# Kernel tuning notes

Hardware: AMD Instinct MI355X
Metric: run time of the kernel (lower is better)

Reference implementation:

```python
import jax, jax.numpy as jnp
import numpy as np
from jax import lax

C_IN, C_OUT, H, W = 64, 128, 512, 512


def setup_inputs() -> dict:
    key = jax.random.key(0)
    k1, k2, k3, k4 = jax.random.split(key, 4)
    x = jax.random.normal(k1, (C_IN, H, W), dtype=jnp.float32)
    # Conv2d params (eqx default: kernel 3x3, bias used). Small init scale for stability.
    conv_w = jax.random.normal(k2, (C_OUT, C_IN, 3, 3), dtype=jnp.float32) * 0.05
    conv_b = jax.random.normal(k3, (C_OUT,), dtype=jnp.float32) * 0.05
    fft_mask = jax.random.normal(k4, (C_OUT, H, W), dtype=jnp.float32)
    return {"x": x, "conv_w": conv_w, "conv_b": conv_b, "fft_mask": fft_mask}


def reference(x, conv_w, conv_b, fft_mask):
    # 3x3 same-padding conv on a single (C,H,W) sample -> (C_OUT,H,W)
    y = lax.conv_general_dilated(
        x[None],  # (1,C_IN,H,W)
        conv_w,
        window_strides=(1, 1),
        padding=((1, 1), (1, 1)),
        dimension_numbers=("NCHW", "OIHW", "NCHW"),
    )[0] + conv_b[:, None, None]
    # Per-channel spectral filter: FFT over (H,W), elementwise complex-mask
    # multiply, inverse FFT, take real part. Vectorized over channels.
    Y = jnp.fft.fftn(y, axes=(1, 2)) * fft_mask
    return jnp.fft.ifftn(Y, axes=(1, 2)).real
```

## Files before the change

kernel.cpp:

```cpp
#include <hip/hip_runtime.h>

#define CIN   64
#define COUT  128
#define HH    512
#define WW    512
#define HW    (HH*WW)

typedef __attribute__((ext_vector_type(8))) short  short8;
typedef __attribute__((ext_vector_type(4))) float  floatx4;


__device__ __forceinline__ unsigned short f2bf(float f) {
    unsigned u = __float_as_uint(f);
    u += 0x7fffu + ((u >> 16) & 1u);
    return (unsigned short)(u >> 16);
}

__device__ __forceinline__ void wave_sync() {
    __builtin_amdgcn_wave_barrier();
    asm volatile("s_waitcnt lgkmcnt(0)" ::: "memory");
    __builtin_amdgcn_sched_barrier(0);
}
template<bool BLK> __device__ __forceinline__ void xsync() {
    if (BLK) __syncthreads(); else wave_sync();
}


__global__ __launch_bounds__(256) void k_wprep(
        const float* __restrict__ cw,
        unsigned short* __restrict__ wt)
{
    int i = blockIdx.x * 256 + threadIdx.x;
    int tap = i >> 13;
    int co  = (i >> 6) & 127;
    int ci  = i & 63;
    wt[i] = f2bf(cw[(co * 64 + ci) * 9 + tap]);
}


__global__ __launch_bounds__(256) void k_xprep(
        const float* __restrict__ x,
        unsigned short* __restrict__ xt)
{
    __shared__ unsigned short tile[64][72];
    int t  = threadIdx.x;
    int h  = blockIdx.x >> 3;
    int w0 = (blockIdx.x & 7) << 6;
    int wl = t & 63;
#pragma unroll
    for (int it = 0; it < 16; ++it) {
        int ci = (t >> 6) + 4 * it;
        tile[wl][ci] = f2bf(x[ci * HW + h * 512 + w0 + wl]);
    }
    __syncthreads();
#pragma unroll
    for (int it = 0; it < 2; ++it) {
        int task = t + 256 * it;
        int w = task >> 3, seg = task & 7;
        *(short8*)&xt[((size_t)(h * 512 + w0 + w)) * 64 + seg * 8] =
            *(const short8*)&tile[w][seg * 8];
    }
}


__global__ __launch_bounds__(256) void k_maskT2(
        const float* __restrict__ mask,
        float* __restrict__ mt)
{
    __shared__ float t1[64][65];
    __shared__ float t2[64][65];
    int b  = blockIdx.x;
    int ch = b >> 6;
    int k0 = ((b >> 3) & 7) << 6;
    int c0 = (b & 7) << 6;
    int t  = threadIdx.x;
    int j  = t & 63, i0 = t >> 6;
    const float* mch = mask + (size_t)ch * HW;
#pragma unroll
    for (int it = 0; it < 16; ++it) {
        int i  = i0 + 4 * it;
        int mi = (512 - (k0 + i)) & 511;
        int mj = (512 - (c0 + j)) & 511;
        t1[i][j] = mch[(size_t)(k0 + i) * 512 + (c0 + j)];
        t2[i][j] = mch[(size_t)mi * 512 + mj];
    }
    __syncthreads();
    float* och = mt + (size_t)ch * HW;
#pragma unroll
    for (int it = 0; it < 16; ++it) {
        int jj = i0 + 4 * it;
        och[(size_t)(c0 + jj) * 512 + k0 + j] = t1[j][jj] + t2[j][jj];
    }
}


__global__ __launch_bounds__(512) void k_conv(
        const unsigned short* __restrict__ xt,
        const unsigned short* __restrict__ wt,
        const float* __restrict__ bias,
        float* __restrict__ y)
{
    __shared__ __align__(16) unsigned short As[3][130][68];

    int b  = blockIdx.x;
    int h  = b >> 2;
    int w0 = (b & 3) << 7;
    int t  = threadIdx.x;
    int lane = t & 63, wv = t >> 6;
    int wm = wv >> 2, wn = wv & 3;
    int l15 = lane & 15, quad = lane >> 4;

    for (int idx = t; idx < 3 * 130 * 8; idx += 512) {
        int dy  = idx / 1040;
        int rem = idx - dy * 1040;
        int p   = rem >> 3, seg = rem & 7;
        int hp  = h + dy - 1;
        int wq  = w0 - 1 + p;
        short8 v = {0, 0, 0, 0, 0, 0, 0, 0};
        if ((unsigned)hp < 512u && (unsigned)wq < 512u)
            v = *(const short8*)&xt[((size_t)(hp * 512 + wq)) * 64 + seg * 8];
        *(short8*)&As[dy][p][seg * 8] = v;
    }
    __syncthreads();

    floatx4 acc[4][2];
#pragma unroll
    for (int mt = 0; mt < 4; ++mt)
#pragma unroll
        for (int nt = 0; nt < 2; ++nt) {
            floatx4 z = {0.f, 0.f, 0.f, 0.f};
            acc[mt][nt] = z;
        }

#pragma unroll
    for (int tap = 0; tap < 9; ++tap) {
        int dy = tap / 3, dx = tap - dy * 3;
        short8 bfr[2][2];
#pragma unroll
        for (int nt = 0; nt < 2; ++nt)
#pragma unroll
            for (int kc = 0; kc < 2; ++kc) {
                int co = wn * 32 + nt * 16 + l15;
                bfr[nt][kc] = *(const short8*)
                    &wt[(tap * 128 + co) * 64 + kc * 32 + quad * 8];
            }
#pragma unroll
        for (int kc = 0; kc < 2; ++kc) {
            int c0 = kc * 32 + quad * 8;
            short8 afr[4];
#pragma unroll
            for (int mt = 0; mt < 4; ++mt) {
                int row = wm * 64 + mt * 16 + l15 + dx;
                afr[mt] = *(const short8*)&As[dy][row][c0];
            }
#pragma unroll
            for (int mt = 0; mt < 4; ++mt)
#pragma unroll
                for (int nt = 0; nt < 2; ++nt)
                    acc[mt][nt] = __builtin_amdgcn_mfma_f32_16x16x32_bf16(
                        afr[mt], bfr[nt][kc], acc[mt][nt], 0, 0, 0);
        }
    }

#pragma unroll
    for (int nt = 0; nt < 2; ++nt) {
        int co = wn * 32 + nt * 16 + l15;
        float bv = bias[co];
#pragma unroll
        for (int mt = 0; mt < 4; ++mt) {
            floatx4 o = acc[mt][nt];
            o[0] += bv; o[1] += bv; o[2] += bv; o[3] += bv;
            int m = wm * 64 + mt * 16 + quad * 4;
            *(floatx4*)&y[co * HW + h * 512 + w0 + m] = o;
        }
    }
}


#define FS 576

__device__ __forceinline__ int slotf(int c, int a) {
    return c * FS + ((a + (a >> 3)) ^ c);
}

__device__ __forceinline__ float2 cadd(float2 a, float2 b){ return make_float2(a.x+b.x, a.y+b.y); }
__device__ __forceinline__ float2 csub(float2 a, float2 b){ return make_float2(a.x-b.x, a.y-b.y); }

template<int DIR> __device__ __forceinline__ float2 twmul(float2 a, float2 t){
    return (DIR > 0) ? make_float2(a.x*t.x - a.y*t.y, a.x*t.y + a.y*t.x)
                     : make_float2(a.x*t.x + a.y*t.y, a.y*t.x - a.x*t.y);
}
template<int DIR> __device__ __forceinline__ float2 mulJ(float2 a){
    return (DIR > 0) ? make_float2(a.y, -a.x) : make_float2(-a.y, a.x);
}

#define RSQRT2 0.70710678118654752f

template<int DIR> __device__ __forceinline__ void dft8(float2* x){
    float2 a0 = cadd(x[0], x[4]), b0 = csub(x[0], x[4]);
    float2 a1 = cadd(x[1], x[5]), b1 = csub(x[1], x[5]);
    float2 a2 = cadd(x[2], x[6]), b2 = csub(x[2], x[6]);
    float2 a3 = cadd(x[3], x[7]), b3 = csub(x[3], x[7]);
    b1 = (DIR > 0) ? make_float2((b1.x + b1.y)*RSQRT2, (b1.y - b1.x)*RSQRT2)
                   : make_float2((b1.x - b1.y)*RSQRT2, (b1.y + b1.x)*RSQRT2);
    b2 = mulJ<DIR>(b2);
    b3 = (DIR > 0) ? make_float2((b3.y - b3.x)*RSQRT2, -(b3.x + b3.y)*RSQRT2)
                   : make_float2(-(b3.x + b3.y)*RSQRT2, (b3.x - b3.y)*RSQRT2);
    float2 c0 = cadd(a0, a2), d0 = csub(a0, a2);
    float2 c1 = cadd(a1, a3), d1 = mulJ<DIR>(csub(a1, a3));
    x[0] = cadd(c0, c1); x[4] = csub(c0, c1);
    x[2] = cadd(d0, d1); x[6] = csub(d0, d1);
    float2 e0 = cadd(b0, b2), f0 = csub(b0, b2);
    float2 e1 = cadd(b1, b3), f1 = mulJ<DIR>(csub(b1, b3));
    x[1] = cadd(e0, e1); x[5] = csub(e0, e1);
    x[3] = cadd(f0, f1); x[7] = csub(f0, f1);
}

template<bool BLK>
__device__ __forceinline__ void fft512_fwd(float2 X[4][8], float2* buf,
                                           const float2* tw, int w, int c) {
#pragma unroll
    for (int b = 0; b < 4; ++b) {
        dft8<1>(X[b]);
        int g = w + 16*b;
#pragma unroll
        for (int k = 1; k < 8; ++k) X[b][k] = twmul<1>(X[b][k], tw[g*k]);
    }
#pragma unroll
    for (int b = 0; b < 4; ++b) {
        int g = w + 16*b;
#pragma unroll
        for (int k = 0; k < 8; ++k) buf[slotf(c, k*64 + g)] = X[b][k];
    }
    xsync<BLK>();
#pragma unroll
    for (int b = 0; b < 4; ++b) {
        int u = w + 16*b; int bs = (u >> 3)*64 + (u & 7);
#pragma unroll
        for (int g2 = 0; g2 < 8; ++g2) X[b][g2] = buf[slotf(c, bs + 8*g2)];
    }
#pragma unroll
    for (int b = 0; b < 4; ++b) {
        dft8<1>(X[b]);
        int g1 = (w + 16*b) & 7;
#pragma unroll
        for (int k = 1; k < 8; ++k) X[b][k] = twmul<1>(X[b][k], tw[8*g1*k]);
    }
    xsync<BLK>();
#pragma unroll
    for (int b = 0; b < 4; ++b) {
        int u = w + 16*b; int bs = (u >> 3)*64 + (u & 7);
#pragma unroll
        for (int k = 0; k < 8; ++k) buf[slotf(c, bs + 8*k)] = X[b][k];
    }
    xsync<BLK>();
#pragma unroll
    for (int b = 0; b < 4; ++b) {
        int v = w + 16*b;
#pragma unroll
        for (int g1 = 0; g1 < 8; ++g1) X[b][g1] = buf[slotf(c, 8*v + g1)];
    }
#pragma unroll
    for (int b = 0; b < 4; ++b) dft8<1>(X[b]);
}

template<bool BLK>
__device__ __forceinline__ void fft512_inv(float2 X[4][8], float2* buf,
                                           const float2* tw, int w, int c) {
#pragma unroll
    for (int b = 0; b < 4; ++b) dft8<-1>(X[b]);
    xsync<BLK>();
#pragma unroll
    for (int b = 0; b < 4; ++b) {
        int v = w + 16*b;
#pragma unroll
        for (int g1 = 0; g1 < 8; ++g1) buf[slotf(c, 8*v + g1)] = X[b][g1];
    }
    xsync<BLK>();
#pragma unroll
    for (int b = 0; b < 4; ++b) {
        int u = w + 16*b; int bs = (u >> 3)*64 + (u & 7);
#pragma unroll
        for (int k = 0; k < 8; ++k) X[b][k] = buf[slotf(c, bs + 8*k)];
    }
#pragma unroll
    for (int b = 0; b < 4; ++b) {
        int g1 = (w + 16*b) & 7;
#pragma unroll
        for (int k = 1; k < 8; ++k) X[b][k] = twmul<-1>(X[b][k], tw[8*g1*k]);
        dft8<-1>(X[b]);
    }
    xsync<BLK>();
#pragma unroll
    for (int b = 0; b < 4; ++b) {
        int u = w + 16*b; int bs = (u >> 3)*64 + (u & 7);
#pragma unroll
        for (int g2 = 0; g2 < 8; ++g2) buf[slotf(c, bs + 8*g2)] = X[b][g2];
    }
    xsync<BLK>();
#pragma unroll
    for (int b = 0; b < 4; ++b) {
        int g = w + 16*b;
#pragma unroll
        for (int k = 0; k < 8; ++k) X[b][k] = buf[slotf(c, k*64 + g)];
    }
#pragma unroll
    for (int b = 0; b < 4; ++b) {
        int g = w + 16*b;
#pragma unroll
        for (int k = 1; k < 8; ++k) X[b][k] = twmul<-1>(X[b][k], tw[g*k]);
        dft8<-1>(X[b]);
    }
}

__device__ __forceinline__ void build_tw(float2* tw, int t) {
    const float a0 = -6.283185307179586f / 512.0f;
    float s, c;
    __sincosf(a0 * (float)t, &s, &c);         tw[t]       = make_float2(c, s);
    __sincosf(a0 * (float)(t + 256), &s, &c); tw[t + 256] = make_float2(c, s);
}


__global__ __launch_bounds__(256) void k_rows_fwd_pair(
        const float* __restrict__ y,
        float2* __restrict__ Z)
{
    __shared__ float2 buf[16 * FS];
    __shared__ float2 tw[512];
    int t = threadIdx.x;
    build_tw(tw, t);
    int c = t >> 4, w = t & 15;
    int p = blockIdx.x >> 5, r0 = (blockIdx.x & 31) << 4;
    const float* yA = y + (size_t)(2*p) * HW;
    const float* yB = yA + HW;

    for (int it = 0; it < 16; ++it) {
        int n = t + 256*it;
        int rr = n >> 8, q = n & 255;
        float2 a2 = *(const float2*)&yA[(size_t)(r0 + rr)*512 + 2*q];
        float2 b2 = *(const float2*)&yB[(size_t)(r0 + rr)*512 + 2*q];
        buf[slotf(rr, 2*q)]     = make_float2(a2.x, b2.x);
        buf[slotf(rr, 2*q + 1)] = make_float2(a2.y, b2.y);
    }
    __syncthreads();
    float2 X[4][8];
#pragma unroll
    for (int b = 0; b < 4; ++b)
#pragma unroll
        for (int r = 0; r < 8; ++r)
            X[b][r] = buf[slotf(c, w + 16*b + 64*r)];
    wave_sync();
    fft512_fwd<false>(X, buf, tw, w, c);

    wave_sync();
#pragma unroll
    for (int b = 0; b < 4; ++b) {
        int v = w + 16*b; int kb = (v >> 3) + 8*(v & 7);
#pragma unroll
        for (int m = 0; m < 8; ++m) buf[slotf(c, kb + 64*m)] = X[b][m];
    }
    __syncthreads();
    size_t zb = (size_t)p * HW + r0;
    for (int it = 0; it < 32; ++it) {
        int n = t + 256*it;
        int col = n >> 4, rr = n & 15;
        Z[zb + (size_t)col*512 + rr] = buf[slotf(rr, col)];
    }
}

__device__ __forceinline__ int col_of(int g, int j) {
    if (g == 0) return (j < 8) ? j : (j == 8 ? 256 : 496 + j);
    return (j < 8) ? 8*g + j : 512 - 8*g - 15 + j;
}
__device__ __forceinline__ int jmir(int g, int j) {
    return (g == 0) ? ((16 - j) & 15) : (15 - j);
}

__global__ __launch_bounds__(256) void k_cols_pair(
        float2* __restrict__ Z,
        const float* __restrict__ mt)
{
    __shared__ float2 buf[16 * FS];
    __shared__ float2 tw[512];
    int t = threadIdx.x;
    build_tw(tw, t);
    int c = t >> 4, w = t & 15;
    int p = blockIdx.x >> 5, g = blockIdx.x & 31;
    int colc = col_of(g, c);
    int cm   = jmir(g, c);
    size_t zch = (size_t)p * HW;
    const float* mAp = mt + (size_t)(2*p) * HW + (size_t)colc * 512;
    const float* mBp = mAp + HW;

    for (int it = 0; it < 32; ++it) {
        int n = t + 256*it;
        int cj = n >> 9, row = n & 511;
        buf[slotf(cj, row)] = Z[zch + (size_t)col_of(g, cj)*512 + row];
    }
    float Sa[4][8], Sb[4][8];
#pragma unroll
    for (int b = 0; b < 4; ++b) {
        int v = w + 16*b; int kb = (v >> 3) + 8*(v & 7);
#pragma unroll
        for (int m = 0; m < 8; ++m) {
            int k1 = kb + 64*m;
            Sa[b][m] = mAp[k1];
            Sb[b][m] = mBp[k1];
        }
    }
    __syncthreads();
    float2 X[4][8];
#pragma unroll
    for (int b = 0; b < 4; ++b)
#pragma unroll
        for (int r = 0; r < 8; ++r)
            X[b][r] = buf[slotf(c, w + 16*b + 64*r)];
    wave_sync();
    fft512_fwd<false>(X, buf, tw, w, c);

    wave_sync();
#pragma unroll
    for (int b = 0; b < 4; ++b) {
        int v = w + 16*b; int kb = (v >> 3) + 8*(v & 7);
#pragma unroll
        for (int m = 0; m < 8; ++m) buf[slotf(c, kb + 64*m)] = X[b][m];
    }
    __syncthreads();

    const float s4 = 0.25f / 262144.0f;
#pragma unroll
    for (int b = 0; b < 4; ++b) {
        int v = w + 16*b; int kb = (v >> 3) + 8*(v & 7);
#pragma unroll
        for (int m = 0; m < 8; ++m) {
            int k1  = kb + 64*m;
            int mk1 = (512 - k1) & 511;
            float2 P = X[b][m];
            float2 Q = buf[slotf(cm, mk1)];
            float alpha = (Sa[b][m] + Sb[b][m]) * s4;
            float beta  = (Sa[b][m] - Sb[b][m]) * s4;
            X[b][m] = make_float2(alpha * P.x + beta * Q.x,
                                  alpha * P.y - beta * Q.y);
        }
    }
    __syncthreads();
    fft512_inv<false>(X, buf, tw, w, c);
    wave_sync();
#pragma unroll
    for (int b = 0; b < 4; ++b)
#pragma unroll
        for (int r = 0; r < 8; ++r)
            buf[slotf(c, w + 16*b + 64*r)] = X[b][r];
    __syncthreads();
    for (int it = 0; it < 32; ++it) {
        int n = t + 256*it;
        int cj = n >> 9, row = n & 511;
        Z[zch + (size_t)col_of(g, cj)*512 + row] = buf[slotf(cj, row)];
    }
}

__global__ __launch_bounds__(256) void k_rows_inv_pair(
        const float2* __restrict__ Z,
        float* __restrict__ out)
{
    __shared__ float2 buf[16 * FS];
    __shared__ float2 tw[512];
    int t = threadIdx.x;
    build_tw(tw, t);
    int c = t >> 4, w = t & 15;
    int p = blockIdx.x >> 5, r0 = (blockIdx.x & 31) << 4;
    size_t zb = (size_t)p * HW + r0;

    for (int it = 0; it < 32; ++it) {
        int n = t + 256*it;
        int col = n >> 4, rr = n & 15;
        buf[slotf(rr, col)] = Z[zb + (size_t)col*512 + rr];
    }
    __syncthreads();

    float2 X[4][8];
#pragma unroll
    for (int b = 0; b < 4; ++b) {
        int v = w + 16*b; int kb = (v >> 3) + 8*(v & 7);
#pragma unroll
        for (int m = 0; m < 8; ++m) X[b][m] = buf[slotf(c, kb + 64*m)];
    }
    fft512_inv<false>(X, buf, tw, w, c);
    wave_sync();
#pragma unroll
    for (int b = 0; b < 4; ++b)
#pragma unroll
        for (int r = 0; r < 8; ++r)
            buf[slotf(c, w + 16*b + 64*r)] = X[b][r];
    __syncthreads();
    float* oA = out + (size_t)(2*p) * HW;
    float* oB = oA + HW;
    for (int it = 0; it < 16; ++it) {
        int n = t + 256*it;
        int rr = n >> 8, q = n & 255;
        float2 v0 = buf[slotf(rr, 2*q)];
        float2 v1 = buf[slotf(rr, 2*q + 1)];
        *(float2*)&oA[(size_t)(r0 + rr)*512 + 2*q] = make_float2(v0.x, v1.x);
        *(float2*)&oB[(size_t)(r0 + rr)*512 + 2*q] = make_float2(v0.y, v1.y);
    }
}


extern "C" void kernel_launch(void* const* d_in, const int* in_sizes, int n_in,
                              void* d_out, int out_size, void* d_ws, size_t ws_size,
                              hipStream_t stream) {
    const float* x    = (const float*)d_in[0];
    const float* cw   = (const float*)d_in[1];
    const float* cb   = (const float*)d_in[2];
    const float* mask = (const float*)d_in[3];

    float*  outRe = (float*)d_out;
    float2* ZT    = (float2*)d_ws;

    unsigned short* xt = (unsigned short*)d_ws;
    unsigned short* wt = (unsigned short*)d_ws + (size_t)HW * 64;

    k_wprep<<<288, 256, 0, stream>>>(cw, wt);
    k_xprep<<<4096, 256, 0, stream>>>(x, xt);
    k_conv<<<2048, 512, 0, stream>>>(xt, wt, cb, outRe);
    k_rows_fwd_pair<<<2048, 256, 0, stream>>>(outRe, ZT);
    k_maskT2<<<8192, 256, 0, stream>>>(mask, outRe);
    k_cols_pair<<<2048, 256, 0, stream>>>(ZT, outRe);
    k_rows_inv_pair<<<2048, 256, 0, stream>>>(ZT, outRe);
}
```

Measured before the change: 631.1 us.

## Halve FFT rows per block and load/store FFT data directly from global memory

The three FFT kernels now give each block 8 rows (32 threads per row, 16 elements per thread) instead of 16, so shared memory and register use per block roughly halve and launch bounds request 4 blocks per CU. The grid doubles to 4096 blocks. The first-stage loads and final stores now go straight between registers and global memory, skipping the shared-memory staging pass where the access pattern allows it. The risks are less coalesced global accesses for the strided per-thread pattern, and more blocks that each rebuild the twiddle table.

```diff
diff --git a/kernel.cpp b/kernel.cpp
--- a/kernel.cpp
+++ b/kernel.cpp
@@ -181,6 +181,9 @@
 
 __device__ __forceinline__ int slotf(int c, int a) {
     return c * FS + ((a + (a >> 3)) ^ c);
+}
+__device__ __forceinline__ int dr6(int v) {
+    return (v >> 3) + 8 * (v & 7);
 }
 
 __device__ __forceinline__ float2 cadd(float2 a, float2 b){ return make_float2(a.x+b.x, a.y+b.y); }
@@ -217,96 +220,96 @@
 }
 
 template<bool BLK>
-__device__ __forceinline__ void fft512_fwd(float2 X[4][8], float2* buf,
+__device__ __forceinline__ void fft512_fwd(float2 X[2][8], float2* buf,
                                            const float2* tw, int w, int c) {
 #pragma unroll
-    for (int b = 0; b < 4; ++b) {
+    for (int b = 0; b < 2; ++b) {
         dft8<1>(X[b]);
-        int g = w + 16*b;
+        int g = w + 32*b;
 #pragma unroll
         for (int k = 1; k < 8; ++k) X[b][k] = twmul<1>(X[b][k], tw[g*k]);
     }
 #pragma unroll
-    for (int b = 0; b < 4; ++b) {
-        int g = w + 16*b;
+    for (int b = 0; b < 2; ++b) {
+        int g = w + 32*b;
 #pragma unroll
         for (int k = 0; k < 8; ++k) buf[slotf(c, k*64 + g)] = X[b][k];
     }
     xsync<BLK>();
 #pragma unroll
-    for (int b = 0; b < 4; ++b) {
-        int u = w + 16*b; int bs = (u >> 3)*64 + (u & 7);
+    for (int b = 0; b < 2; ++b) {
+        int u = w + 32*b; int bs = (u >> 3)*64 + (u & 7);
 #pragma unroll
         for (int g2 = 0; g2 < 8; ++g2) X[b][g2] = buf[slotf(c, bs + 8*g2)];
     }
 #pragma unroll
-    for (int b = 0; b < 4; ++b) {
+    for (int b = 0; b < 2; ++b) {
         dft8<1>(X[b]);
-        int g1 = (w + 16*b) & 7;
+        int g1 = (w + 32*b) & 7;
 #pragma unroll
         for (int k = 1; k < 8; ++k) X[b][k] = twmul<1>(X[b][k], tw[8*g1*k]);
     }
     xsync<BLK>();
 #pragma unroll
-    for (int b = 0; b < 4; ++b) {
-        int u = w + 16*b; int bs = (u >> 3)*64 + (u & 7);
+    for (int b = 0; b < 2; ++b) {
+        int u = w + 32*b; int bs = (u >> 3)*64 + (u & 7);
 #pragma unroll
         for (int k = 0; k < 8; ++k) buf[slotf(c, bs + 8*k)] = X[b][k];
     }
     xsync<BLK>();
 #pragma unroll
-    for (int b = 0; b < 4; ++b) {
-        int v = w + 16*b;
+    for (int b = 0; b < 2; ++b) {
+        int v = w + 32*b;
 #pragma unroll
         for (int g1 = 0; g1 < 8; ++g1) X[b][g1] = buf[slotf(c, 8*v + g1)];
     }
 #pragma unroll
-    for (int b = 0; b < 4; ++b) dft8<1>(X[b]);
+    for (int b = 0; b < 2; ++b) dft8<1>(X[b]);
 }
 
 template<bool BLK>
-__device__ __forceinline__ void fft512_inv(float2 X[4][8], float2* buf,
+__device__ __forceinline__ void fft512_inv(float2 X[2][8], float2* buf,
                                            const float2* tw, int w, int c) {
 #pragma unroll
-    for (int b = 0; b < 4; ++b) dft8<-1>(X[b]);
-    xsync<BLK>();
-#pragma unroll
-    for (int b = 0; b < 4; ++b) {
-        int v = w + 16*b;
+    for (int b = 0; b < 2; ++b) dft8<-1>(X[b]);
+    xsync<BLK>();
+#pragma unroll
+    for (int b = 0; b < 2; ++b) {
+        int v = w + 32*b;
 #pragma unroll
         for (int g1 = 0; g1 < 8; ++g1) buf[slotf(c, 8*v + g1)] = X[b][g1];
     }
     xsync<BLK>();
 #pragma unroll
-    for (int b = 0; b < 4; ++b) {
-        int u = w + 16*b; int bs = (u >> 3)*64 + (u & 7);
+    for (int b = 0; b < 2; ++b) {
+        int u = w + 32*b; int bs = (u >> 3)*64 + (u & 7);
 #pragma unroll
         for (int k = 0; k < 8; ++k) X[b][k] = buf[slotf(c, bs + 8*k)];
     }
 #pragma unroll
-    for (int b = 0; b < 4; ++b) {
-        int g1 = (w + 16*b) & 7;
+    for (int b = 0; b < 2; ++b) {
+        int g1 = (w + 32*b) & 7;
 #pragma unroll
         for (int k = 1; k < 8; ++k) X[b][k] = twmul<-1>(X[b][k], tw[8*g1*k]);
         dft8<-1>(X[b]);
     }
     xsync<BLK>();
 #pragma unroll
-    for (int b = 0; b < 4; ++b) {
-        int u = w + 16*b; int bs = (u >> 3)*64 + (u & 7);
+    for (int b = 0; b < 2; ++b) {
+        int u = w + 32*b; int bs = (u >> 3)*64 + (u & 7);
 #pragma unroll
         for (int g2 = 0; g2 < 8; ++g2) buf[slotf(c, bs + 8*g2)] = X[b][g2];
     }
     xsync<BLK>();
 #pragma unroll
-    for (int b = 0; b < 4; ++b) {
-        int g = w + 16*b;
+    for (int b = 0; b < 2; ++b) {
+        int g = w + 32*b;
 #pragma unroll
         for (int k = 0; k < 8; ++k) X[b][k] = buf[slotf(c, k*64 + g)];
     }
 #pragma unroll
-    for (int b = 0; b < 4; ++b) {
-        int g = w + 16*b;
+    for (int b = 0; b < 2; ++b) {
+        int g = w + 32*b;
 #pragma unroll
         for (int k = 1; k < 8; ++k) X[b][k] = twmul<-1>(X[b][k], tw[g*k]);
         dft8<-1>(X[b]);
@@ -321,86 +324,80 @@
 }
 
 
-__global__ __launch_bounds__(256) void k_rows_fwd_pair(
+__global__ __launch_bounds__(256, 4) void k_rows_fwd_pair(
         const float* __restrict__ y,
         float2* __restrict__ Z)
 {
-    __shared__ float2 buf[16 * FS];
+    __shared__ float2 buf[8 * FS];
     __shared__ float2 tw[512];
     int t = threadIdx.x;
     build_tw(tw, t);
-    int c = t >> 4, w = t & 15;
-    int p = blockIdx.x >> 5, r0 = (blockIdx.x & 31) << 4;
-    const float* yA = y + (size_t)(2*p) * HW;
+    int c = t >> 5, w = t & 31;
+    int p = blockIdx.x >> 6, r0 = (blockIdx.x & 63) << 3;
+    const float* yA = y + (size_t)(2*p) * HW + (size_t)(r0 + c) * 512;
     const float* yB = yA + HW;
 
+    float2 X[2][8];
+#pragma unroll
+    for (int b = 0; b < 2; ++b)
+#pragma unroll
+        for (int r = 0; r < 8; ++r) {
+            int off = w + 32*b + 64*r;
+            X[b][r] = make_float2(yA[off], yB[off]);
+        }
+    __syncthreads();
+    fft512_fwd<false>(X, buf, tw, w, c);
+
+    wave_sync();
+#pragma unroll
+    for (int b = 0; b < 2; ++b) {
+        int kb = dr6(w + 32*b);
+#pragma unroll
+        for (int m = 0; m < 8; ++m) buf[slotf(c, kb + 64*m)] = X[b][m];
+    }
+    __syncthreads();
+    size_t zb = (size_t)p * HW + r0;
     for (int it = 0; it < 16; ++it) {
         int n = t + 256*it;
-        int rr = n >> 8, q = n & 255;
-        float2 a2 = *(const float2*)&yA[(size_t)(r0 + rr)*512 + 2*q];
-        float2 b2 = *(const float2*)&yB[(size_t)(r0 + rr)*512 + 2*q];
-        buf[slotf(rr, 2*q)]     = make_float2(a2.x, b2.x);
-        buf[slotf(rr, 2*q + 1)] = make_float2(a2.y, b2.y);
-    }
-    __syncthreads();
-    float2 X[4][8];
-#pragma unroll
-    for (int b = 0; b < 4; ++b)
-#pragma unroll
-        for (int r = 0; r < 8; ++r)
-            X[b][r] = buf[slotf(c, w + 16*b + 64*r)];
-    wave_sync();
-    fft512_fwd<false>(X, buf, tw, w, c);
-
-    wave_sync();
-#pragma unroll
-    for (int b = 0; b < 4; ++b) {
-        int v = w + 16*b; int kb = (v >> 3) + 8*(v & 7);
-#pragma unroll
-        for (int m = 0; m < 8; ++m) buf[slotf(c, kb + 64*m)] = X[b][m];
-    }
-    __syncthreads();
-    size_t zb = (size_t)p * HW + r0;
-    for (int it = 0; it < 32; ++it) {
-        int n = t + 256*it;
-        int col = n >> 4, rr = n & 15;
+        int col = n >> 3, rr = n & 7;
         Z[zb + (size_t)col*512 + rr] = buf[slotf(rr, col)];
     }
 }
 
 __device__ __forceinline__ int col_of(int g, int j) {
-    if (g == 0) return (j < 8) ? j : (j == 8 ? 256 : 496 + j);
-    return (j < 8) ? 8*g + j : 512 - 8*g - 15 + j;
+    if (g == 0) return (j < 4) ? j : (j == 4 ? 256 : 504 + j);
+    return (j < 4) ? 4*g + j : 512 - 4*g - 7 + j;
 }
 __device__ __forceinline__ int jmir(int g, int j) {
-    return (g == 0) ? ((16 - j) & 15) : (15 - j);
-}
-
-__global__ __launch_bounds__(256) void k_cols_pair(
+    return (g == 0) ? ((8 - j) & 7) : (7 - j);
+}
+
+__global__ __launch_bounds__(256, 4) void k_cols_pair(
         float2* __restrict__ Z,
         const float* __restrict__ mt)
 {
-    __shared__ float2 buf[16 * FS];
+    __shared__ float2 buf[8 * FS];
     __shared__ float2 tw[512];
     int t = threadIdx.x;
     build_tw(tw, t);
-    int c = t >> 4, w = t & 15;
-    int p = blockIdx.x >> 5, g = blockIdx.x & 31;
+    int c = t >> 5, w = t & 31;
+    int p = blockIdx.x >> 6, g = blockIdx.x & 63;
     int colc = col_of(g, c);
     int cm   = jmir(g, c);
-    size_t zch = (size_t)p * HW;
+    size_t zcol = (size_t)p * HW + (size_t)colc * 512;
     const float* mAp = mt + (size_t)(2*p) * HW + (size_t)colc * 512;
     const float* mBp = mAp + HW;
 
-    for (int it = 0; it < 32; ++it) {
-        int n = t + 256*it;
-        int cj = n >> 9, row = n & 511;
-        buf[slotf(cj, row)] = Z[zch + (size_t)col_of(g, cj)*512 + row];
-    }
-    float Sa[4][8], Sb[4][8];
-#pragma unroll
-    for (int b = 0; b < 4; ++b) {
-        int v = w + 16*b; int kb = (v >> 3) + 8*(v & 7);
+    float2 X[2][8];
+#pragma unroll
+    for (int b = 0; b < 2; ++b)
+#pragma unroll
+        for (int r = 0; r < 8; ++r)
+            X[b][r] = Z[zcol + w + 32*b + 64*r];
+    float Sa[2][8], Sb[2][8];
+#pragma unroll
+    for (int b = 0; b < 2; ++b) {
+        int kb = dr6(w + 32*b);
 #pragma unroll
         for (int m = 0; m < 8; ++m) {
             int k1 = kb + 64*m;
@@ -409,19 +406,12 @@
         }
     }
     __syncthreads();
-    float2 X[4][8];
-#pragma unroll
-    for (int b = 0; b < 4; ++b)
-#pragma unroll
-        for (int r = 0; r < 8; ++r)
-            X[b][r] = buf[slotf(c, w + 16*b + 64*r)];
+    fft512_fwd<false>(X, buf, tw, w, c);
+
     wave_sync();
-    fft512_fwd<false>(X, buf, tw, w, c);
-
-    wave_sync();
-#pragma unroll
-    for (int b = 0; b < 4; ++b) {
-        int v = w + 16*b; int kb = (v >> 3) + 8*(v & 7);
+#pragma unroll
+    for (int b = 0; b < 2; ++b) {
+        int kb = dr6(w + 32*b);
 #pragma unroll
         for (int m = 0; m < 8; ++m) buf[slotf(c, kb + 64*m)] = X[b][m];
     }
@@ -429,8 +419,8 @@
 
     const float s4 = 0.25f / 262144.0f;
 #pragma unroll
-    for (int b = 0; b < 4; ++b) {
-        int v = w + 16*b; int kb = (v >> 3) + 8*(v & 7);
+    for (int b = 0; b < 2; ++b) {
+        int kb = dr6(w + 32*b);
 #pragma unroll
         for (int m = 0; m < 8; ++m) {
             int k1  = kb + 64*m;
@@ -445,64 +435,51 @@
     }
     __syncthreads();
     fft512_inv<false>(X, buf, tw, w, c);
-    wave_sync();
-#pragma unroll
-    for (int b = 0; b < 4; ++b)
+#pragma unroll
+    for (int b = 0; b < 2; ++b)
 #pragma unroll
         for (int r = 0; r < 8; ++r)
-            buf[slotf(c, w + 16*b + 64*r)] = X[b][r];
-    __syncthreads();
-    for (int it = 0; it < 32; ++it) {
-        int n = t + 256*it;
-        int cj = n >> 9, row = n & 511;
-        Z[zch + (size_t)col_of(g, cj)*512 + row] = buf[slotf(cj, row)];
-    }
-}
-
-__global__ __launch_bounds__(256) void k_rows_inv_pair(
+            Z[zcol + w + 32*b + 64*r] = X[b][r];
+}
+
+__global__ __launch_bounds__(256, 4) void k_rows_inv_pair(
         const float2* __restrict__ Z,
         float* __restrict__ out)
 {
-    __shared__ float2 buf[16 * FS];
+    __shared__ float2 buf[8 * FS];
     __shared__ float2 tw[512];
     int t = threadIdx.x;
     build_tw(tw, t);
-    int c = t >> 4, w = t & 15;
-    int p = blockIdx.x >> 5, r0 = (blockIdx.x & 31) << 4;
+    int c = t >> 5, w = t & 31;
+    int p = blockIdx.x >> 6, r0 = (blockIdx.x & 63) << 3;
     size_t zb = (size_t)p * HW + r0;
 
-    for (int it = 0; it < 32; ++it) {
-        int n = t + 256*it;
-        int col = n >> 4, rr = n & 15;
-        buf[slotf(rr, col)] = Z[zb + (size_t)col*512 + rr];
-    }
-    __syncthreads();
-
-    float2 X[4][8];
-#pragma unroll
-    for (int b = 0; b < 4; ++b) {
-        int v = w + 16*b; int kb = (v >> 3) + 8*(v & 7);
-#pragma unroll
-        for (int m = 0; m < 8; ++m) X[b][m] = buf[slotf(c, kb + 64*m)];
-    }
-    fft512_inv<false>(X, buf, tw, w, c);
-    wave_sync();
-#pragma unroll
-    for (int b = 0; b < 4; ++b)
-#pragma unroll
-        for (int r = 0; r < 8; ++r)
-            buf[slotf(c, w + 16*b + 64*r)] = X[b][r];
-    __syncthreads();
-    float* oA = out + (size_t)(2*p) * HW;
-    float* oB = oA + HW;
     for (int it = 0; it < 16; ++it) {
         int n = t + 256*it;
-        int rr = n >> 8, q = n & 255;
-        float2 v0 = buf[slotf(rr, 2*q)];
-        float2 v1 = buf[slotf(rr, 2*q + 1)];
-        *(float2*)&oA[(size_t)(r0 + rr)*512 + 2*q] = make_float2(v0.x, v1.x);
-        *(float2*)&oB[(size_t)(r0 + rr)*512 + 2*q] = make_float2(v0.y, v1.y);
-    }
+        int col = n >> 3, rr = n & 7;
+        buf[slotf(rr, col)] = Z[zb + (size_t)col*512 + rr];
+    }
+    __syncthreads();
+
+    float2 X[2][8];
+#pragma unroll
+    for (int b = 0; b < 2; ++b) {
+        int kb = dr6(w + 32*b);
+#pragma unroll
+        for (int m = 0; m < 8; ++m) X[b][m] = buf[slotf(c, kb + 64*m)];
+    }
+    fft512_inv<false>(X, buf, tw, w, c);
+
+    float* oA = out + (size_t)(2*p) * HW + (size_t)(r0 + c) * 512;
+    float* oB = oA + HW;
+#pragma unroll
+    for (int b = 0; b < 2; ++b)
+#pragma unroll
+        for (int r = 0; r < 8; ++r) {
+            int off = w + 32*b + 64*r;
+            oA[off] = X[b][r].x;
+            oB[off] = X[b][r].y;
+        }
 }
 
 
@@ -523,8 +500,8 @@
     k_wprep<<<288, 256, 0, stream>>>(cw, wt);
     k_xprep<<<4096, 256, 0, stream>>>(x, xt);
     k_conv<<<2048, 512, 0, stream>>>(xt, wt, cb, outRe);
-    k_rows_fwd_pair<<<2048, 256, 0, stream>>>(outRe, ZT);
+    k_rows_fwd_pair<<<4096, 256, 0, stream>>>(outRe, ZT);
     k_maskT2<<<8192, 256, 0, stream>>>(mask, outRe);
-    k_cols_pair<<<2048, 256, 0, stream>>>(ZT, outRe);
-    k_rows_inv_pair<<<2048, 256, 0, stream>>>(ZT, outRe);
-}
+    k_cols_pair<<<4096, 256, 0, stream>>>(ZT, outRe);
+    k_rows_inv_pair<<<4096, 256, 0, stream>>>(ZT, outRe);
+}
```

Result: slower. 659.5 us (+4.5%).
